# Kernel optimization log

Measured on AMD Instinct MI355X. Metric: run time of the kernel, lower is better.

The kernel has to match this reference:

```python
import jax, jax.numpy as jnp
import numpy as np

B, N, D, E, FF_MULT = 2, 1024, 1024, 8, 4
H = D * FF_MULT


def setup_inputs() -> dict:
    key = jax.random.key(0)
    k = jax.random.split(key, 6)
    tokens = jax.random.normal(k[0], (B, N, D), dtype=jnp.float32)
    # uniform(0,1): strictly positive -> every expert processes every token
    dispatch_weights = jax.random.uniform(k[1], (B, N, E), dtype=jnp.float32)
    combine_weights = jax.random.uniform(k[2], (B, N, E), dtype=jnp.float32)
    # per-expert SwiGLU params, stacked on leading expert axis.
    # stored pre-transposed: y = x @ W  (torch Linear weight is [out,in])
    xavier_dh = np.sqrt(2.0 / (D + H))
    Wg = jax.random.normal(k[3], (E, D, H), dtype=jnp.float32) * xavier_dh
    Wv = jax.random.normal(k[4], (E, D, H), dtype=jnp.float32) * xavier_dh
    Wo = jax.random.normal(k[5], (E, H, D), dtype=jnp.float32) * (0.02 * xavier_dh)
    scale = jnp.full((E,), 1.0 / E, dtype=jnp.float32)  # output_scale init 1/E
    return {"tokens": tokens, "dispatch_weights": dispatch_weights,
            "combine_weights": combine_weights, "Wg": Wg, "Wv": Wv,
            "Wo": Wo, "scale": scale}


def reference(tokens, dispatch_weights, combine_weights, Wg, Wv, Wo, scale):
    b, n, d = tokens.shape
    x = tokens.reshape(b * n, d)                      # (T, D)
    disp = dispatch_weights.reshape(b * n, E)         # (T, E)
    comb = combine_weights.reshape(b * n, E)          # (T, E)
    # SwiGLU FFN for all experts at once (dense grouped GEMM)
    gate = jax.nn.gelu(jnp.einsum('td,edh->teh', x, Wg), approximate=False)
    value = jnp.einsum('td,edh->teh', x, Wv)
    expert_out = jnp.einsum('teh,ehd->ted', gate * value, Wo)  # (T, E, D)
    expert_out = expert_out * scale[None, :, None]
    # combine: weight by combine_weights where dispatched (dispatch > 0)
    w = jnp.where(disp > 0, comb, 0.0)                # (T, E)
    output = jnp.einsum('ted,te->td', expert_out, w)
    return output.reshape(b, n, d)
```

## Files before the change

kernel.cpp:

```cpp
#include <hip/hip_runtime.h>
#include <math.h>

#define T_TOK 2048
#define DDIM 1024
#define HDIM 4096
#define NEXP 8
#define NPRIME 8192
#define KTOT (NEXP * HDIM)
#define NSPLIT 8

typedef unsigned short u16;
typedef __attribute__((ext_vector_type(4))) float f32x4;
typedef __attribute__((ext_vector_type(8))) __bf16 bf16x8;
typedef __attribute__((ext_vector_type(8))) unsigned short u16x8;
typedef __attribute__((ext_vector_type(4))) unsigned short u16x4;

__device__ __forceinline__ u16 f2bf(float f) {
  unsigned int u = __builtin_bit_cast(unsigned int, f);
  u += 0x7fffu + ((u >> 16) & 1u);
  return (u16)(u >> 16);
}

__device__ __forceinline__ void stage16(const u16* g, u16* l) {
  __builtin_amdgcn_global_load_lds((__attribute__((address_space(1))) void*)g,
                                   (__attribute__((address_space(3))) void*)l,
                                   16, 0, 0);
}

__global__ void cvt_x_kernel(const float* __restrict__ x, u16* __restrict__ xb) {
  int i = (blockIdx.x * 256 + threadIdx.x) * 8;
  float4 a = *(const float4*)(x + i);
  float4 b = *(const float4*)(x + i + 4);
  u16x8 o;
  o[0] = f2bf(a.x); o[1] = f2bf(a.y); o[2] = f2bf(a.z); o[3] = f2bf(a.w);
  o[4] = f2bf(b.x); o[5] = f2bf(b.y); o[6] = f2bf(b.z); o[7] = f2bf(b.w);
  *(u16x8*)(xb + i) = o;
}

__global__ void transpose_all_kernel(const float* __restrict__ Wg,
                                     const float* __restrict__ Wv,
                                     const float* __restrict__ Wo,
                                     u16* __restrict__ wgvT, u16* __restrict__ woT2) {
  __shared__ float lds[64][65];
  const int bid = blockIdx.x;
  const int e = bid / 3072;
  const int r = bid % 3072;
  const int which = r >> 10;
  const int tt = r & 1023;
  const float* src; int R, C;
  if (which == 2) { src = Wo + (size_t)e * HDIM * DDIM; R = HDIM; C = DDIM; }
  else            { src = (which ? Wv : Wg) + (size_t)e * DDIM * HDIM; R = DDIM; C = HDIM; }
  const int nrt = R >> 6;
  const int r0 = (tt % nrt) << 6, c0 = (tt / nrt) << 6;
  const int tid = threadIdx.x;
#pragma unroll
  for (int i = 0; i < 4; ++i) {
    int f4 = tid + 256 * i;
    int row = f4 >> 4, c4 = (f4 & 15) << 2;
    float4 v = *(const float4*)(src + (size_t)(r0 + row) * C + c0 + c4);
    lds[row][c4] = v.x; lds[row][c4 + 1] = v.y; lds[row][c4 + 2] = v.z; lds[row][c4 + 3] = v.w;
  }
  __syncthreads();
#pragma unroll
  for (int i = 0; i < 4; ++i) {
    int f4 = tid + 256 * i;
    int cc = f4 >> 4, r4 = (f4 & 15) << 2;
    u16x4 o;
    o[0] = f2bf(lds[r4][cc]);     o[1] = f2bf(lds[r4 + 1][cc]);
    o[2] = f2bf(lds[r4 + 2][cc]); o[3] = f2bf(lds[r4 + 3][cc]);
    u16* dst;
    if (which == 2) {
      dst = woT2 + (size_t)(c0 + cc) * KTOT + e * HDIM + r0 + r4;
    } else {
      int h = c0 + cc;
      int rowp = ((h >> 4) << 5) + which * 16 + (h & 15);
      dst = wgvT + (size_t)e * NPRIME * DDIM + (size_t)rowp * DDIM + r0 + r4;
    }
    *(u16x4*)dst = o;
  }
}


template<int KS>
__device__ __forceinline__ void gemm_loop(const u16* Ab, const u16* Bb,
                                          int Am0, int Bn0, int kbase, int NT,
                                          u16* lds, int tid, f32x4 (&acc)[8][4]) {
  const int lane = tid & 63;
  const int wave = tid >> 6;
  const int wm = wave >> 2, wn = wave & 3;
  const int l15 = lane & 15, lkq = lane >> 4;

  const int sl = tid & 7, rw = tid >> 3;
  const int slx = (sl ^ (rw & 7)) << 3;
  const int rb = (rw & 31) + ((rw >> 5) << 6);
  const u16* pA = Ab + (size_t)(Am0 + rw) * KS + kbase + slx;
  const u16* pB = Bb + (size_t)(Bn0 + rb) * KS + kbase + slx;
  const int dA = rw * 64 + sl * 8;
  const int dB = 16384 + rb * 64 + sl * 8;

  auto SA0 = [&](int k, u16* slot) {
    stage16(pA + k, slot + dA);
    stage16(pA + (size_t)128 * KS + k, slot + dA + 128 * 64);
  };
  auto SA1 = [&](int k, u16* slot) {
    stage16(pA + (size_t)64 * KS + k, slot + dA + 64 * 64);
    stage16(pA + (size_t)192 * KS + k, slot + dA + 192 * 64);
  };
  auto SB0 = [&](int k, u16* slot) {
    stage16(pB + k, slot + dB);
    stage16(pB + (size_t)128 * KS + k, slot + dB + 128 * 64);
  };
  auto SB1 = [&](int k, u16* slot) {
    stage16(pB + (size_t)32 * KS + k, slot + dB + 32 * 64);
    stage16(pB + (size_t)160 * KS + k, slot + dB + 160 * 64);
  };

  const int swz0 = (lkq ^ (l15 & 7)) << 3;
  const int swz1 = ((4 | lkq) ^ (l15 & 7)) << 3;
  const int arow = (wm * 128 + l15) * 64;
  const int brow = 16384 + (wn * 64 + l15) * 64;
  const int a0 = arow + swz0, a1 = arow + swz1;
  const int b0 = brow + swz0, b1 = brow + swz1;

  SA0(0, lds); SB0(0, lds); SB1(0, lds); SA1(0, lds);
  asm volatile("s_waitcnt vmcnt(4)" ::: "memory");
  __builtin_amdgcn_s_barrier();

#pragma unroll 1
  for (int t = 0; t < NT; ++t) {
    const u16* s = lds + (t & 1) * 32768;
    u16* s2 = lds + ((t & 1) ^ 1) * 32768;
    const int kn = (t + 1) << 6;
    const bool more = (t + 1 < NT);
    bf16x8 af[4][2], bfr[4][2];

#pragma unroll
    for (int mf = 0; mf < 4; ++mf) {
      af[mf][0] = *(const bf16x8*)(s + a0 + mf * 1024);
      af[mf][1] = *(const bf16x8*)(s + a1 + mf * 1024);
    }
#pragma unroll
    for (int nf = 0; nf < 2; ++nf) {
      bfr[nf][0] = *(const bf16x8*)(s + b0 + nf * 1024);
      bfr[nf][1] = *(const bf16x8*)(s + b1 + nf * 1024);
    }
    if (more) SA0(kn, s2);
    __builtin_amdgcn_sched_barrier(0);
    __builtin_amdgcn_s_barrier();
    asm volatile("s_waitcnt lgkmcnt(0)" ::: "memory");
    __builtin_amdgcn_sched_barrier(0);
    __builtin_amdgcn_s_setprio(1);
#pragma unroll
    for (int ks = 0; ks < 2; ++ks)
#pragma unroll
      for (int mf = 0; mf < 4; ++mf)
#pragma unroll
        for (int nf = 0; nf < 2; ++nf)
          acc[mf][nf] = __builtin_amdgcn_mfma_f32_16x16x32_bf16(af[mf][ks], bfr[nf][ks], acc[mf][nf], 0, 0, 0);
    __builtin_amdgcn_s_setprio(0);
    if (more) { asm volatile("s_waitcnt vmcnt(4)" ::: "memory"); }
    else      { asm volatile("s_waitcnt vmcnt(2)" ::: "memory"); }
    __builtin_amdgcn_s_barrier();
    __builtin_amdgcn_sched_barrier(0);

#pragma unroll
    for (int nf = 2; nf < 4; ++nf) {
      bfr[nf][0] = *(const bf16x8*)(s + b0 + nf * 1024);
      bfr[nf][1] = *(const bf16x8*)(s + b1 + nf * 1024);
    }
    if (more) SB0(kn, s2);
    __builtin_amdgcn_sched_barrier(0);
    __builtin_amdgcn_s_barrier();
    asm volatile("s_waitcnt lgkmcnt(0)" ::: "memory");
    __builtin_amdgcn_sched_barrier(0);
    __builtin_amdgcn_s_setprio(1);
#pragma unroll
    for (int ks = 0; ks < 2; ++ks)
#pragma unroll
      for (int mf = 0; mf < 4; ++mf)
#pragma unroll
        for (int nf = 2; nf < 4; ++nf)
          acc[mf][nf] = __builtin_amdgcn_mfma_f32_16x16x32_bf16(af[mf][ks], bfr[nf][ks], acc[mf][nf], 0, 0, 0);
    __builtin_amdgcn_s_setprio(0);
    if (more) { asm volatile("s_waitcnt vmcnt(4)" ::: "memory"); }
    else      { asm volatile("s_waitcnt vmcnt(0)" ::: "memory"); }
    __builtin_amdgcn_s_barrier();
    __builtin_amdgcn_sched_barrier(0);

#pragma unroll
    for (int mf = 0; mf < 4; ++mf) {
      af[mf][0] = *(const bf16x8*)(s + a0 + 4096 + mf * 1024);
      af[mf][1] = *(const bf16x8*)(s + a1 + 4096 + mf * 1024);
    }
    if (more) SB1(kn, s2);
    __builtin_amdgcn_sched_barrier(0);
    __builtin_amdgcn_s_barrier();
    asm volatile("s_waitcnt lgkmcnt(0)" ::: "memory");
    __builtin_amdgcn_sched_barrier(0);
    __builtin_amdgcn_s_setprio(1);
#pragma unroll
    for (int ks = 0; ks < 2; ++ks)
#pragma unroll
      for (int mf = 0; mf < 4; ++mf)
#pragma unroll
        for (int nf = 0; nf < 2; ++nf)
          acc[4 + mf][nf] = __builtin_amdgcn_mfma_f32_16x16x32_bf16(af[mf][ks], bfr[nf][ks], acc[4 + mf][nf], 0, 0, 0);
    __builtin_amdgcn_s_setprio(0);
    __builtin_amdgcn_s_barrier();
    __builtin_amdgcn_sched_barrier(0);

    if (more) SA1(kn, s2);
    __builtin_amdgcn_s_setprio(1);
#pragma unroll
    for (int ks = 0; ks < 2; ++ks)
#pragma unroll
      for (int mf = 0; mf < 4; ++mf)
#pragma unroll
        for (int nf = 2; nf < 4; ++nf)
          acc[4 + mf][nf] = __builtin_amdgcn_mfma_f32_16x16x32_bf16(af[mf][ks], bfr[nf][ks], acc[4 + mf][nf], 0, 0, 0);
    __builtin_amdgcn_s_setprio(0);
    if (more) { asm volatile("s_waitcnt vmcnt(4)" ::: "memory"); }
    __builtin_amdgcn_s_barrier();
    __builtin_amdgcn_sched_barrier(0);
  }
}

__global__ void __launch_bounds__(512, 2)
gemm_gv_kernel(const u16* __restrict__ xb, const u16* __restrict__ wgvT,
               const float* __restrict__ disp, const float* __restrict__ comb,
               const float* __restrict__ scale, u16* __restrict__ h) {
  __shared__ u16 lds[65536];

  const int bid = blockIdx.x;
  const int wg = (bid & 7) * 256 + (bid >> 3);
  const int e  = wg >> 8;
  const int rr = wg & 255;
  const int nt = rr >> 3;
  const int mt = rr & 7;

  const int tid = threadIdx.x;
  const int lane = tid & 63;
  const int wave = tid >> 6;
  const int wm = wave >> 2, wn = wave & 3;
  const int l15 = lane & 15, lkq = lane >> 4;

  const u16* Bb = wgvT + (size_t)e * NPRIME * DDIM;
  const int Am0 = mt * 256;
  const int Bn0 = nt * 256;

  f32x4 acc[8][4] = {};
  gemm_loop<DDIM>(xb, Bb, Am0, Bn0, 0, DDIM / 64, lds, tid, acc);

  const float s_e = scale[e];
  const int hbase = nt * 128 + wn * 32;
#pragma unroll
  for (int a = 0; a < 8; ++a) {
#pragma unroll
    for (int r = 0; r < 4; ++r) {
      const int t = Am0 + wm * 128 + a * 16 + lkq * 4 + r;
      const float dv = disp[t * NEXP + e];
      const float cv = comb[t * NEXP + e];
      const float s = (dv > 0.0f) ? cv * s_e : 0.0f;
#pragma unroll
      for (int jj = 0; jj < 2; ++jj) {
        const float g = acc[a][2 * jj][r];
        const float v = acc[a][2 * jj + 1][r];
        const float ge = 0.5f * g * (1.0f + erff(g * 0.70710678f));
        h[(size_t)t * KTOT + e * HDIM + hbase + jj * 16 + l15] = f2bf(ge * v * s);
      }
    }
  }
}

__global__ void __launch_bounds__(512, 2)
gemm_out_kernel(const u16* __restrict__ hb, const u16* __restrict__ woT2,
                float* __restrict__ P) {
  __shared__ u16 lds[65536];

  const int bid = blockIdx.x;
  const int wg = (bid & 7) * 32 + (bid >> 3);
  const int kz = wg >> 5;
  const int rr = wg & 31;
  const int nt = rr >> 3;
  const int mt = rr & 7;

  const int tid = threadIdx.x;
  const int lane = tid & 63;
  const int wave = tid >> 6;
  const int wm = wave >> 2, wn = wave & 3;
  const int l15 = lane & 15, lkq = lane >> 4;

  const int Am0 = mt * 256;
  const int Bn0 = nt * 256;
  const int kbase = kz * (KTOT / NSPLIT);

  f32x4 acc[8][4] = {};
  gemm_loop<KTOT>(hb, woT2, Am0, Bn0, kbase, (KTOT / NSPLIT) / 64, lds, tid, acc);

  float* Pp = P + (size_t)kz * (T_TOK * DDIM);
#pragma unroll
  for (int a = 0; a < 8; ++a) {
#pragma unroll
    for (int r = 0; r < 4; ++r) {
      const int t = Am0 + wm * 128 + a * 16 + lkq * 4 + r;
#pragma unroll
      for (int nf = 0; nf < 4; ++nf)
        Pp[(size_t)t * DDIM + Bn0 + wn * 64 + nf * 16 + l15] = acc[a][nf][r];
    }
  }
}

__global__ void reduce_out_kernel(const float* __restrict__ P, float* __restrict__ out) {
  int i = blockIdx.x * 256 + threadIdx.x;
  float4 a = ((const float4*)P)[i];
#pragma unroll
  for (int s = 1; s < NSPLIT; ++s) {
    float4 b = ((const float4*)P)[i + s * (T_TOK * DDIM / 4)];
    a.x += b.x; a.y += b.y; a.z += b.z; a.w += b.w;
  }
  ((float4*)out)[i] = a;
}

extern "C" void kernel_launch(void* const* d_in, const int* in_sizes, int n_in,
                              void* d_out, int out_size, void* d_ws, size_t ws_size,
                              hipStream_t stream) {
  const float* tokens = (const float*)d_in[0];
  const float* disp   = (const float*)d_in[1];
  const float* comb   = (const float*)d_in[2];
  const float* Wg     = (const float*)d_in[3];
  const float* Wv     = (const float*)d_in[4];
  const float* Wo     = (const float*)d_in[5];
  const float* scale  = (const float*)d_in[6];
  float* out = (float*)d_out;

  char* ws = (char*)d_ws;
  const size_t MB = 1024 * 1024;
  u16* xb    = (u16*)(ws);
  u16* wgvT  = (u16*)(ws + 4   * MB);
  u16* woT2  = (u16*)(ws + 132 * MB);
  u16* hbuf  = (u16*)(ws + 196 * MB);
  float* P   = (float*)(ws + 324 * MB);

  cvt_x_kernel<<<1024, 256, 0, stream>>>(tokens, xb);
  transpose_all_kernel<<<24576, 256, 0, stream>>>(Wg, Wv, Wo, wgvT, woT2);
  gemm_gv_kernel<<<2048, 512, 0, stream>>>(xb, wgvT, disp, comb, scale, hbuf);
  gemm_out_kernel<<<256, 512, 0, stream>>>(hbuf, woT2, P);
  reduce_out_kernel<<<2048, 256, 0, stream>>>(P, out);
}
```

Before: 553.0 us.

## Deepen GEMM global-to-LDS prefetch to two tiles ahead within double buffer

After: 549.0 us. No clear change (-0.7%).

```diff
diff --git a/kernel.cpp b/kernel.cpp
--- a/kernel.cpp
+++ b/kernel.cpp
@@ -98,22 +98,19 @@
   const int dA = rw * 64 + sl * 8;
   const int dB = 16384 + rb * 64 + sl * 8;
 
-  auto SA0 = [&](int k, u16* slot) {
-    stage16(pA + k, slot + dA);
-    stage16(pA + (size_t)128 * KS + k, slot + dA + 128 * 64);
-  };
-  auto SA1 = [&](int k, u16* slot) {
-    stage16(pA + (size_t)64 * KS + k, slot + dA + 64 * 64);
-    stage16(pA + (size_t)192 * KS + k, slot + dA + 192 * 64);
-  };
-  auto SB0 = [&](int k, u16* slot) {
-    stage16(pB + k, slot + dB);
-    stage16(pB + (size_t)128 * KS + k, slot + dB + 128 * 64);
-  };
-  auto SB1 = [&](int k, u16* slot) {
-    stage16(pB + (size_t)32 * KS + k, slot + dB + 32 * 64);
-    stage16(pB + (size_t)160 * KS + k, slot + dB + 160 * 64);
-  };
+  auto slot = [&](int t) -> u16* { return lds + (t & 1) * 32768; };
+  auto SA0 = [&](int t) { u16* sp = slot(t); const int k = t << 6;
+    stage16(pA + k, sp + dA);
+    stage16(pA + (size_t)128 * KS + k, sp + dA + 8192); };
+  auto SA1 = [&](int t) { u16* sp = slot(t); const int k = t << 6;
+    stage16(pA + (size_t)64 * KS + k, sp + dA + 4096);
+    stage16(pA + (size_t)192 * KS + k, sp + dA + 12288); };
+  auto SB0 = [&](int t) { u16* sp = slot(t); const int k = t << 6;
+    stage16(pB + k, sp + dB);
+    stage16(pB + (size_t)128 * KS + k, sp + dB + 8192); };
+  auto SB1 = [&](int t) { u16* sp = slot(t); const int k = t << 6;
+    stage16(pB + (size_t)32 * KS + k, sp + dB + 2048);
+    stage16(pB + (size_t)160 * KS + k, sp + dB + 10240); };
 
   const int swz0 = (lkq ^ (l15 & 7)) << 3;
   const int swz1 = ((4 | lkq) ^ (l15 & 7)) << 3;
@@ -122,16 +119,16 @@
   const int a0 = arow + swz0, a1 = arow + swz1;
   const int b0 = brow + swz0, b1 = brow + swz1;
 
-  SA0(0, lds); SB0(0, lds); SB1(0, lds); SA1(0, lds);
-  asm volatile("s_waitcnt vmcnt(4)" ::: "memory");
+  SA0(0); SB0(0); SB1(0); SA1(0);
+  SA0(1); SB0(1); SB1(1);
+  asm volatile("s_waitcnt vmcnt(10)" ::: "memory");
   __builtin_amdgcn_s_barrier();
 
 #pragma unroll 1
   for (int t = 0; t < NT; ++t) {
-    const u16* s = lds + (t & 1) * 32768;
-    u16* s2 = lds + ((t & 1) ^ 1) * 32768;
-    const int kn = (t + 1) << 6;
-    const bool more = (t + 1 < NT);
+    const u16* s = slot(t);
+    const int tp1 = (t + 1 < NT) ? t + 1 : NT - 1;
+    const int tp2 = (t + 2 < NT) ? t + 2 : NT - 1;
     bf16x8 af[4][2], bfr[4][2];
 
 #pragma unroll
@@ -144,8 +141,8 @@
       bfr[nf][0] = *(const bf16x8*)(s + b0 + nf * 1024);
       bfr[nf][1] = *(const bf16x8*)(s + b1 + nf * 1024);
     }
-    if (more) SA0(kn, s2);
-    __builtin_amdgcn_sched_barrier(0);
+    SA1(tp1);
+    asm volatile("s_waitcnt vmcnt(10)" ::: "memory");
     __builtin_amdgcn_s_barrier();
     asm volatile("s_waitcnt lgkmcnt(0)" ::: "memory");
     __builtin_amdgcn_sched_barrier(0);
@@ -158,18 +155,15 @@
         for (int nf = 0; nf < 2; ++nf)
           acc[mf][nf] = __builtin_amdgcn_mfma_f32_16x16x32_bf16(af[mf][ks], bfr[nf][ks], acc[mf][nf], 0, 0, 0);
     __builtin_amdgcn_s_setprio(0);
-    if (more) { asm volatile("s_waitcnt vmcnt(4)" ::: "memory"); }
-    else      { asm volatile("s_waitcnt vmcnt(2)" ::: "memory"); }
-    __builtin_amdgcn_s_barrier();
-    __builtin_amdgcn_sched_barrier(0);
+    __builtin_amdgcn_s_barrier();
 
 #pragma unroll
     for (int nf = 2; nf < 4; ++nf) {
       bfr[nf][0] = *(const bf16x8*)(s + b0 + nf * 1024);
       bfr[nf][1] = *(const bf16x8*)(s + b1 + nf * 1024);
     }
-    if (more) SB0(kn, s2);
-    __builtin_amdgcn_sched_barrier(0);
+    SA0(tp2);
+    asm volatile("s_waitcnt vmcnt(10)" ::: "memory");
     __builtin_amdgcn_s_barrier();
     asm volatile("s_waitcnt lgkmcnt(0)" ::: "memory");
     __builtin_amdgcn_sched_barrier(0);
@@ -182,18 +176,14 @@
         for (int nf = 2; nf < 4; ++nf)
           acc[mf][nf] = __builtin_amdgcn_mfma_f32_16x16x32_bf16(af[mf][ks], bfr[nf][ks], acc[mf][nf], 0, 0, 0);
     __builtin_amdgcn_s_setprio(0);
-    if (more) { asm volatile("s_waitcnt vmcnt(4)" ::: "memory"); }
-    else      { asm volatile("s_waitcnt vmcnt(0)" ::: "memory"); }
-    __builtin_amdgcn_s_barrier();
-    __builtin_amdgcn_sched_barrier(0);
+    __builtin_amdgcn_s_barrier();
 
 #pragma unroll
     for (int mf = 0; mf < 4; ++mf) {
       af[mf][0] = *(const bf16x8*)(s + a0 + 4096 + mf * 1024);
       af[mf][1] = *(const bf16x8*)(s + a1 + 4096 + mf * 1024);
     }
-    if (more) SB1(kn, s2);
-    __builtin_amdgcn_sched_barrier(0);
+    SB0(tp2);
     __builtin_amdgcn_s_barrier();
     asm volatile("s_waitcnt lgkmcnt(0)" ::: "memory");
     __builtin_amdgcn_sched_barrier(0);
@@ -207,9 +197,10 @@
           acc[4 + mf][nf] = __builtin_amdgcn_mfma_f32_16x16x32_bf16(af[mf][ks], bfr[nf][ks], acc[4 + mf][nf], 0, 0, 0);
     __builtin_amdgcn_s_setprio(0);
     __builtin_amdgcn_s_barrier();
-    __builtin_amdgcn_sched_barrier(0);
-
-    if (more) SA1(kn, s2);
+
+    SB1(tp2);
+    asm volatile("s_waitcnt vmcnt(10)" ::: "memory");
+    __builtin_amdgcn_s_barrier();
     __builtin_amdgcn_s_setprio(1);
 #pragma unroll
     for (int ks = 0; ks < 2; ++ks)
@@ -219,9 +210,7 @@
         for (int nf = 2; nf < 4; ++nf)
           acc[4 + mf][nf] = __builtin_amdgcn_mfma_f32_16x16x32_bf16(af[mf][ks], bfr[nf][ks], acc[4 + mf][nf], 0, 0, 0);
     __builtin_amdgcn_s_setprio(0);
-    if (more) { asm volatile("s_waitcnt vmcnt(4)" ::: "memory"); }
-    __builtin_amdgcn_s_barrier();
-    __builtin_amdgcn_sched_barrier(0);
+    __builtin_amdgcn_s_barrier();
   }
 }
 
```
